# Kernel optimization log

Hardware: AMD Instinct MI355X
Metric: run time of the kernel (lower is better)

## Reference

```python
import jax, jax.numpy as jnp
import numpy as np
import math

N_MOD = 4
# ordered pairs (src, dst), src != dst, in the original nested-loop order
PAIRS = [(s, d) for s in range(N_MOD) for d in range(N_MOD) if s != d]
SRC = np.array([s for s, d in PAIRS])
DST = np.array([d for s, d in PAIRS])


def setup_inputs() -> dict:
    key = jax.random.key(0)
    k0, k1, k2, k3 = jax.random.split(key, 4)
    B, D = 2048, 1024
    x = jax.random.normal(k0, (N_MOD, B, D), dtype=jnp.float32)
    # xavier_uniform with gain=0.1 -> small weights; emulate scale
    W = jax.random.normal(k1, (len(PAIRS), D, D), dtype=jnp.float32) * 0.005
    local_freq = jax.random.uniform(k2, (N_MOD, D), dtype=jnp.float32, minval=8.0, maxval=12.0)
    global_freq = jax.random.uniform(k3, (N_MOD,), dtype=jnp.float32, minval=0.5, maxval=4.0)
    strength = jnp.full((N_MOD,), 0.1, dtype=jnp.float32)
    return {"x": x, "W": W, "local_freq": local_freq,
            "global_freq": global_freq, "strength": strength, "current_clk": 5}


def reference(x, W, local_freq, global_freq, strength, current_clk):
    # x: [4, B, D] stacked module outputs; W: [12, D_dst, D_src]
    src = jnp.asarray(SRC)
    dst = jnp.asarray(DST)
    # nn.Linear (no bias): y = x @ W.T  -> grouped GEMM over all 12 pairs
    y = jnp.einsum('pbi,poi->pbo', x[src], W)          # [12, B, D]
    out = jax.ops.segment_sum(y, dst, num_segments=N_MOD)  # [4, B, D]

    # interference pattern: strength * (sin(2*pi*f_local*t) + sin(2*pi*f_global*t))
    t = 2.0 * math.pi * current_clk * 0.001
    local = jnp.sin(t * local_freq)[:, None, :]        # [4, 1, D]
    glob = jnp.sin(t * global_freq)[:, None, None]     # [4, 1, 1]
    out = out + strength[:, None, None] * (local + glob)
    return out
```

## Files before the change

### kernel.cpp

```cpp
#include <hip/hip_runtime.h>
#include <cstdint>
#include <cstddef>


typedef _Float16 f16;
typedef _Float16 f16x8 __attribute__((ext_vector_type(8)));
typedef _Float16 f16x4 __attribute__((ext_vector_type(4)));
typedef float    f32x4 __attribute__((ext_vector_type(4)));

#define NMOD  4
#define BROWS 2048
#define DDIM  1024
#define BK    32
#define NT    96

__global__ void cvt_f32_f16(const float* __restrict__ in, f16* __restrict__ out, int n4) {
    int i = blockIdx.x * blockDim.x + threadIdx.x;
    if (i >= n4) return;
    float4 v = reinterpret_cast<const float4*>(in)[i];
    f16x4 h = { (f16)v.x, (f16)v.y, (f16)v.z, (f16)v.w };
    reinterpret_cast<f16x4*>(out)[i] = h;
}

__global__ void bias_kernel(const float* __restrict__ lf, const float* __restrict__ gf,
                            const float* __restrict__ st, const int* __restrict__ clk,
                            float* __restrict__ bias) {
    int d = blockIdx.x;
    int o = threadIdx.x;
    float t = (float)(6.283185307179586 * 0.001 * (double)(*clk));
    bias[d * DDIM + o] = st[d] * (sinf(t * lf[d * DDIM + o]) + sinf(t * gf[d]));
}

__device__ __forceinline__ void g2l16(const f16* g, f16* l) {
    __builtin_amdgcn_global_load_lds(
        (const __attribute__((address_space(1))) void*)g,
        (__attribute__((address_space(3))) void*)l,
        16, 0, 0);
}

__global__ __launch_bounds__(256, 2)
void gemm_kernel(const f16* __restrict__ X,
                 const f16* __restrict__ Wh,
                 const float* __restrict__ bias,
                 float* __restrict__ out) {
    __shared__ f16 As[2][128 * BK];
    __shared__ f16 Bs[2][128 * BK];

    const int bid = blockIdx.x;
    const int swz = ((bid & 7) << 6) + (bid >> 3);
    const int d  = swz >> 7;
    const int m0 = ((swz >> 3) & 15) << 7;
    const int n0 = (swz & 7) << 7;

    const int t  = threadIdx.x;
    const int l  = t & 63;
    const int w  = t >> 6;
    const int wr = w >> 1;
    const int wc = w & 1;
    const int fr = l & 15;
    const int fq = l >> 4;

    const int srow = (w << 4) + (l >> 2);
    const int scol = (l & 3) << 3;

    f32x4 acc[4][4] = {};

    auto stage = [&](int b, int tt) {
        const int j  = tt >> 5;
        const int k0 = (tt & 31) << 5;
        const int s  = j + (j >= d ? 1 : 0);
        const int p  = s * 3 + d - (d > s ? 1 : 0);
        const f16* xa = X  + ((size_t)s * BROWS + m0 + srow) * DDIM + k0 + scol;
        const f16* xb = Wh + ((size_t)p * DDIM  + n0 + srow) * DDIM + k0 + scol;
        f16* lA = &As[b][w << 9];
        f16* lB = &Bs[b][w << 9];
        g2l16(xa,                     lA);
        g2l16(xa + (size_t)64 * DDIM, lA + 2048);
        g2l16(xb,                     lB);
        g2l16(xb + (size_t)64 * DDIM, lB + 2048);
    };

    auto compute = [&](int b) {
        f16x8 af[4], bf[4];
        #pragma unroll
        for (int m = 0; m < 4; ++m)
            af[m] = *reinterpret_cast<const f16x8*>(&As[b][(wr * 64 + m * 16 + fr) * BK + fq * 8]);
        #pragma unroll
        for (int n = 0; n < 4; ++n)
            bf[n] = *reinterpret_cast<const f16x8*>(&Bs[b][(wc * 64 + n * 16 + fr) * BK + fq * 8]);
        #pragma unroll
        for (int m = 0; m < 4; ++m)
            #pragma unroll
            for (int n = 0; n < 4; ++n)
                acc[m][n] = __builtin_amdgcn_mfma_f32_16x16x32_f16(af[m], bf[n], acc[m][n], 0, 0, 0);
    };

    stage(0, 0);
    __syncthreads();

    #pragma unroll 1
    for (int tt = 0; tt < NT - 2; tt += 2) {
        stage(1, tt + 1);
        compute(0);
        __syncthreads();
        stage(0, tt + 2);
        compute(1);
        __syncthreads();
    }
    stage(1, NT - 1);
    compute(0);
    __syncthreads();
    compute(1);

    const int c0 = n0 + wc * 64 + fr;
    const int r0 = m0 + wr * 64 + fq * 4;
    float* od = out + (size_t)d * BROWS * DDIM;
    const float* bd = bias + d * DDIM;
    #pragma unroll
    for (int n = 0; n < 4; ++n) {
        const float bv = bd[c0 + n * 16];
        #pragma unroll
        for (int m = 0; m < 4; ++m) {
            #pragma unroll
            for (int r = 0; r < 4; ++r) {
                od[(size_t)(r0 + m * 16 + r) * DDIM + (c0 + n * 16)] = acc[m][n][r] + bv;
            }
        }
    }
}

__global__ __launch_bounds__(256)
void gemm_f32_fallback(const float* __restrict__ X, const float* __restrict__ W,
                       const float* __restrict__ lf, const float* __restrict__ gf,
                       const float* __restrict__ st, const int* __restrict__ clk,
                       float* __restrict__ out) {
    const int d = blockIdx.y;
    const int b = blockIdx.x;
    __shared__ float xs[3][DDIM];
    for (int j = 0; j < 3; ++j) {
        int s = j + (j >= d ? 1 : 0);
        for (int i = threadIdx.x; i < DDIM; i += 256)
            xs[j][i] = X[((size_t)s * BROWS + b) * DDIM + i];
    }
    __syncthreads();
    float t = (float)(6.283185307179586 * 0.001 * (double)(*clk));
    for (int oi = 0; oi < 4; ++oi) {
        int o = threadIdx.x + oi * 256;
        float acc = 0.f;
        for (int j = 0; j < 3; ++j) {
            int s = j + (j >= d ? 1 : 0);
            int p = s * 3 + d - (d > s ? 1 : 0);
            const float* wrow = W + ((size_t)p * DDIM + o) * DDIM;
            float a = 0.f;
            for (int k = 0; k < DDIM; k += 4) {
                float4 wv = *reinterpret_cast<const float4*>(wrow + k);
                a += xs[j][k] * wv.x + xs[j][k + 1] * wv.y
                   + xs[j][k + 2] * wv.z + xs[j][k + 3] * wv.w;
            }
            acc += a;
        }
        out[((size_t)d * BROWS + b) * DDIM + o] =
            acc + st[d] * (sinf(t * lf[d * DDIM + o]) + sinf(t * gf[d]));
    }
}

extern "C" void kernel_launch(void* const* d_in, const int* in_sizes, int n_in,
                              void* d_out, int out_size, void* d_ws, size_t ws_size,
                              hipStream_t stream) {
    const float* x  = (const float*)d_in[0];
    const float* W  = (const float*)d_in[1];
    const float* lf = (const float*)d_in[2];
    const float* gf = (const float*)d_in[3];
    const float* st = (const float*)d_in[4];
    const int*  clk = (const int*)d_in[5];
    float* out = (float*)d_out;

    const size_t need = ((size_t)40 << 20) + 16384;
    if (ws_size < need) {
        gemm_f32_fallback<<<dim3(BROWS, NMOD), dim3(256), 0, stream>>>(x, W, lf, gf, st, clk, out);
        return;
    }

    f16*   x16  = (f16*)d_ws;
    f16*   w16  = (f16*)((char*)d_ws + ((size_t)16 << 20));
    float* bias = (float*)((char*)d_ws + ((size_t)40 << 20));

    cvt_f32_f16<<<dim3(8192),  dim3(256), 0, stream>>>(x, x16, 8388608 / 4);
    cvt_f32_f16<<<dim3(12288), dim3(256), 0, stream>>>(W, w16, 12582912 / 4);
    bias_kernel<<<dim3(NMOD), dim3(1024), 0, stream>>>(lf, gf, st, clk, bias);
    gemm_kernel<<<dim3(512), dim3(256), 0, stream>>>(x16, w16, bias, out);
}
```

Baseline: 203.6 us.

## Shrink GEMM N-tile, swizzle LDS, fuse bias into epilogue and merge conversions

Merges the two f32->f16 conversion kernels into one launch and computes the sinusoidal bias directly in the GEMM epilogue, dropping the bias kernel and buffer. The GEMM tile is halved in N (128x64) with double the blocks and higher occupancy target. An XOR swizzle is applied to the LDS layout via the lane-to-address mapping of global_load_lds and matched on reads to reduce bank conflicts. The smaller tile lowers data reuse per block and risks mismatched swizzle correctness.

```diff
diff --git a/kernel.cpp b/kernel.cpp
--- a/kernel.cpp
+++ b/kernel.cpp
@@ -14,21 +14,15 @@
 #define BK    32
 #define NT    96
 
-__global__ void cvt_f32_f16(const float* __restrict__ in, f16* __restrict__ out, int n4) {
+__global__ void cvt_all(const float* __restrict__ x, const float* __restrict__ W,
+                        f16* __restrict__ out16) {
     int i = blockIdx.x * blockDim.x + threadIdx.x;
-    if (i >= n4) return;
-    float4 v = reinterpret_cast<const float4*>(in)[i];
+    const int nx4 = 8388608 / 4;
+    float4 v;
+    if (i < nx4) v = reinterpret_cast<const float4*>(x)[i];
+    else         v = reinterpret_cast<const float4*>(W)[i - nx4];
     f16x4 h = { (f16)v.x, (f16)v.y, (f16)v.z, (f16)v.w };
-    reinterpret_cast<f16x4*>(out)[i] = h;
-}
-
-__global__ void bias_kernel(const float* __restrict__ lf, const float* __restrict__ gf,
-                            const float* __restrict__ st, const int* __restrict__ clk,
-                            float* __restrict__ bias) {
-    int d = blockIdx.x;
-    int o = threadIdx.x;
-    float t = (float)(6.283185307179586 * 0.001 * (double)(*clk));
-    bias[d * DDIM + o] = st[d] * (sinf(t * lf[d * DDIM + o]) + sinf(t * gf[d]));
+    reinterpret_cast<f16x4*>(out16)[i] = h;
 }
 
 __device__ __forceinline__ void g2l16(const f16* g, f16* l) {
@@ -38,19 +32,22 @@
         16, 0, 0);
 }
 
-__global__ __launch_bounds__(256, 2)
+__global__ __launch_bounds__(256, 4)
 void gemm_kernel(const f16* __restrict__ X,
                  const f16* __restrict__ Wh,
-                 const float* __restrict__ bias,
+                 const float* __restrict__ lf,
+                 const float* __restrict__ gf,
+                 const float* __restrict__ st,
+                 const int*  __restrict__ clk,
                  float* __restrict__ out) {
     __shared__ f16 As[2][128 * BK];
-    __shared__ f16 Bs[2][128 * BK];
+    __shared__ f16 Bs[2][64 * BK];
 
     const int bid = blockIdx.x;
-    const int swz = ((bid & 7) << 6) + (bid >> 3);
-    const int d  = swz >> 7;
-    const int m0 = ((swz >> 3) & 15) << 7;
-    const int n0 = (swz & 7) << 7;
+    const int swz = ((bid & 7) << 7) | (bid >> 3);
+    const int d  = swz >> 8;
+    const int m0 = ((swz >> 4) & 15) << 7;
+    const int n0 = (swz & 15) << 6;
 
     const int t  = threadIdx.x;
     const int l  = t & 63;
@@ -60,10 +57,13 @@
     const int fr = l & 15;
     const int fq = l >> 4;
 
-    const int srow = (w << 4) + (l >> 2);
-    const int scol = (l & 3) << 3;
+    const int g    = (w * 64 + l) ^ ((l >> 3) & 7);
+    const int srow = g >> 2;
+    const int scol = (g & 3) << 3;
 
-    f32x4 acc[4][4] = {};
+    const int arx = (fr >> 1) << 3;
+
+    f32x4 acc[4][2] = {};
 
     auto stage = [&](int b, int tt) {
         const int j  = tt >> 5;
@@ -77,21 +77,22 @@
         g2l16(xa,                     lA);
         g2l16(xa + (size_t)64 * DDIM, lA + 2048);
         g2l16(xb,                     lB);
-        g2l16(xb + (size_t)64 * DDIM, lB + 2048);
     };
 
     auto compute = [&](int b) {
-        f16x8 af[4], bf[4];
+        f16x8 af[4], bf[2];
         #pragma unroll
         for (int m = 0; m < 4; ++m)
-            af[m] = *reinterpret_cast<const f16x8*>(&As[b][(wr * 64 + m * 16 + fr) * BK + fq * 8]);
+            af[m] = *reinterpret_cast<const f16x8*>(
+                &As[b][(((wr * 64 + m * 16 + fr) * BK) + fq * 8) ^ arx]);
         #pragma unroll
-        for (int n = 0; n < 4; ++n)
-            bf[n] = *reinterpret_cast<const f16x8*>(&Bs[b][(wc * 64 + n * 16 + fr) * BK + fq * 8]);
+        for (int n = 0; n < 2; ++n)
+            bf[n] = *reinterpret_cast<const f16x8*>(
+                &Bs[b][(((wc * 32 + n * 16 + fr) * BK) + fq * 8) ^ arx]);
         #pragma unroll
         for (int m = 0; m < 4; ++m)
             #pragma unroll
-            for (int n = 0; n < 4; ++n)
+            for (int n = 0; n < 2; ++n)
                 acc[m][n] = __builtin_amdgcn_mfma_f32_16x16x32_f16(af[m], bf[n], acc[m][n], 0, 0, 0);
     };
 
@@ -112,13 +113,15 @@
     __syncthreads();
     compute(1);
 
-    const int c0 = n0 + wc * 64 + fr;
+    const int c0 = n0 + wc * 32 + fr;
     const int r0 = m0 + wr * 64 + fq * 4;
+    const float tt_ = (float)(6.283185307179586 * 0.001 * (double)(*clk));
+    const float sd  = st[d];
+    const float sgf = sinf(tt_ * gf[d]);
     float* od = out + (size_t)d * BROWS * DDIM;
-    const float* bd = bias + d * DDIM;
     #pragma unroll
-    for (int n = 0; n < 4; ++n) {
-        const float bv = bd[c0 + n * 16];
+    for (int n = 0; n < 2; ++n) {
+        const float bv = sd * (sinf(tt_ * lf[d * DDIM + c0 + n * 16]) + sgf);
         #pragma unroll
         for (int m = 0; m < 4; ++m) {
             #pragma unroll
@@ -175,18 +178,15 @@
     const int*  clk = (const int*)d_in[5];
     float* out = (float*)d_out;
 
-    const size_t need = ((size_t)40 << 20) + 16384;
+    const size_t need = (size_t)40 << 20;
     if (ws_size < need) {
         gemm_f32_fallback<<<dim3(BROWS, NMOD), dim3(256), 0, stream>>>(x, W, lf, gf, st, clk, out);
         return;
     }
 
-    f16*   x16  = (f16*)d_ws;
-    f16*   w16  = (f16*)((char*)d_ws + ((size_t)16 << 20));
-    float* bias = (float*)((char*)d_ws + ((size_t)40 << 20));
+    f16* x16 = (f16*)d_ws;
+    f16* w16 = (f16*)((char*)d_ws + ((size_t)16 << 20));
 
-    cvt_f32_f16<<<dim3(8192),  dim3(256), 0, stream>>>(x, x16, 8388608 / 4);
-    cvt_f32_f16<<<dim3(12288), dim3(256), 0, stream>>>(W, w16, 12582912 / 4);
-    bias_kernel<<<dim3(NMOD), dim3(1024), 0, stream>>>(lf, gf, st, clk, bias);
-    gemm_kernel<<<dim3(512), dim3(256), 0, stream>>>(x16, w16, bias, out);
+    cvt_all<<<dim3(20480), dim3(256), 0, stream>>>(x, W, x16);
+    gemm_kernel<<<dim3(1024), dim3(256), 0, stream>>>(x16, w16, lf, gf, st, clk, out);
 }
```

Result: no change. 202.4 us (-0.6%).
